# Kernel tuning notes

Hardware: AMD Instinct MI355X
Metric: run time of the kernel (lower is better)

The kernel has to match this reference:

```python
import jax, jax.numpy as jnp
import numpy as np

B, T, V, D, E = 128, 50, 10000, 512, 2048


def setup_inputs() -> dict:
    key = jax.random.key(0)
    ks = jax.random.split(key, 14)
    s = 1.0 / np.sqrt(D)
    enc_out = jax.random.normal(ks[0], (B, E), jnp.float32)
    captions = jax.random.randint(ks[1], (B, T), 0, V)
    caplens = jax.random.randint(ks[2], (B, 1), 2, T + 1)
    caplens = caplens.at[0, 0].set(T)  # ensure max(caplens)-1 == T-1 (static shape)
    return {
        "enc_out": enc_out,
        "captions": captions,
        "caplens": caplens,
        "emb_W": jax.random.normal(ks[3], (V, D), jnp.float32),
        "W_ih": jax.random.uniform(ks[4], (4 * D, D), jnp.float32, -s, s),
        "W_hh": jax.random.uniform(ks[5], (4 * D, D), jnp.float32, -s, s),
        "b_ih": jax.random.uniform(ks[6], (4 * D,), jnp.float32, -s, s),
        "b_hh": jax.random.uniform(ks[7], (4 * D,), jnp.float32, -s, s),
        "fc_W": jax.random.uniform(ks[8], (V, D), jnp.float32, -s, s),
        "fc_b": jnp.zeros((V,), jnp.float32),
        "init_h_W": jax.random.uniform(ks[9], (D, E), jnp.float32, -s, s),
        "init_h_b": jnp.zeros((D,), jnp.float32),
        "init_c_W": jax.random.uniform(ks[10], (D, E), jnp.float32, -s, s),
        "init_c_b": jnp.zeros((D,), jnp.float32),
    }


def reference(enc_out, captions, caplens, emb_W, W_ih, W_hh, b_ih, b_hh,
              fc_W, fc_b, init_h_W, init_h_b, init_c_W, init_c_b):
    # Sort by caption length, descending (manual packing in the torch code).
    cl = caplens[:, 0]
    sort_idx = jnp.argsort(-cl)
    cl = cl[sort_idx]
    enc = enc_out[sort_idx]
    caps = captions[sort_idx]

    # init_states
    h0 = enc @ init_h_W.T + init_h_b  # [B, D]
    c0 = enc @ init_c_W.T + init_c_b

    emb = emb_W[caps]                  # [B, T, D] embedding gather
    dec_lens = cl - 1                  # decode lengths, max == T-1 by construction
    Tm = caps.shape[1] - 1             # static max timesteps

    # active-row mask per timestep: row b is active at step t iff t < dec_lens[b]
    masks = jnp.arange(Tm)[:, None] < dec_lens[None, :]   # [Tm, B]
    xs = jnp.moveaxis(emb[:, :Tm, :], 1, 0)               # [Tm, B, D]

    def step(carry, inp):
        h, c = carry
        x_t, m = inp                                      # [B,D], [B]
        gates = x_t @ W_ih.T + b_ih + h @ W_hh.T + b_hh   # [B, 4D]
        i, f, g, o = jnp.split(gates, 4, axis=-1)
        i = jax.nn.sigmoid(i)
        f = jax.nn.sigmoid(f)
        g = jnp.tanh(g)
        o = jax.nn.sigmoid(o)
        c_new = f * c + i * g
        h_new = o * jnp.tanh(c_new)
        mm = m[:, None]
        # inactive (shorter) rows keep their old state; torch never touches them
        h = jnp.where(mm, h_new, h)
        c = jnp.where(mm, c_new, c)
        # dropout in eval mode == identity; preds only written for active rows
        preds = jnp.where(mm, h_new @ fc_W.T + fc_b, 0.0)  # [B, V]
        return (h, c), preds

    (_, _), preds = jax.lax.scan(step, (h0, c0), (xs, masks))  # [Tm, B, V]
    predictions = jnp.moveaxis(preds, 0, 1)                    # [B, Tm, V]
    return predictions, caps, dec_lens, sort_idx
```

## Files before the change

kernel.cpp:

```cpp
#include <hip/hip_runtime.h>
#include <hip/hip_bf16.h>
#include <math.h>

typedef __attribute__((ext_vector_type(8))) short short8;
typedef __attribute__((ext_vector_type(4))) float f32x4;
typedef __attribute__((ext_vector_type(4))) unsigned short us4;
typedef unsigned short u16;
typedef unsigned long long u64;

#define TM 49
#define NV 10000
#define NLSTM 64
#define NFC 192
#define SMEM_BYTES 133184

__device__ __forceinline__ u16 f2bf(float f) {
    union { float f; unsigned u; } v; v.f = f;
    unsigned r = v.u + 0x7fffu + ((v.u >> 16) & 1u);
    return (u16)(r >> 16);
}
__device__ __forceinline__ float fsigm(float x) {
    return 1.0f / (1.0f + __expf(-x));
}
__device__ __forceinline__ float ftanh(float x) {
    float x2 = fminf(fmaxf(x + x, -30.0f), 30.0f);
    float e = __expf(x2);
    return (e - 1.0f) / (e + 1.0f);
}

__device__ __forceinline__ short8 ld_cp128(const u16* p) {
    short8 r;
    asm volatile("global_load_dwordx4 %0, %1, off sc0 sc1" : "=v"(r) : "v"(p));
    return r;
}
__device__ __forceinline__ void st_cp16(u16* p, unsigned v) {
    asm volatile("global_store_short %0, %1, off sc0 sc1" :: "v"(p), "v"(v) : "memory");
}
__device__ __forceinline__ void st_cp32f(float* p, float v) {
    asm volatile("global_store_dword %0, %1, off sc0 sc1" :: "v"(p), "v"(v) : "memory");
}
__device__ __forceinline__ unsigned ld_cp32_wait(const unsigned* p) {
    unsigned r;
    asm volatile("global_load_dword %0, %1, off sc0 sc1\n\ts_waitcnt vmcnt(0)"
                 : "=v"(r) : "v"(p) : "memory");
    return r;
}

__global__ __launch_bounds__(128) void k_sort(
    const int* __restrict__ caplens, const int* __restrict__ captions,
    const float* __restrict__ bih, const float* __restrict__ bhh,
    int* __restrict__ sidx, int* __restrict__ decl, int* __restrict__ capsS,
    float* __restrict__ bsum, float* __restrict__ out_tail,
    unsigned* __restrict__ slots, unsigned* __restrict__ xcnt,
    int* __restrict__ offs, int* __restrict__ rowmap, int* __restrict__ maskmap)
{
    __shared__ int s_cl[128];
    __shared__ int s_si[128];
    __shared__ int s_dl[128];
    __shared__ int s_n[49];
    __shared__ int s_off[50];
    __shared__ int s_moff[128];
    int tid = threadIdx.x;
    for (int k = tid; k < 256; k += 128)
        __hip_atomic_store(&slots[k], 0u, __ATOMIC_RELAXED, __HIP_MEMORY_SCOPE_AGENT);
    for (int k = tid; k < 1568; k += 128)
        __hip_atomic_store(&xcnt[k], 0u, __ATOMIC_RELAXED, __HIP_MEMORY_SCOPE_AGENT);
    int my = caplens[tid];
    s_cl[tid] = my;
    __syncthreads();
    int r = 0;
    for (int j = 0; j < 128; j++) {
        int cj = s_cl[j];
        if (cj > my || (cj == my && j < tid)) r++;
    }
    s_si[r] = tid;
    __syncthreads();
    int src = s_si[tid];
    sidx[tid] = src;
    int dl = s_cl[src] - 1;
    decl[tid] = dl;
    s_dl[tid] = dl;
    out_tail[6400 + tid] = (float)dl;
    out_tail[6528 + tid] = (float)src;
    for (int t = 0; t < 50; t++) {
        int tok = captions[src * 50 + t];
        capsS[tid * 50 + t] = tok;
        out_tail[tid * 50 + t] = (float)tok;
    }
    for (int k = tid; k < 2048; k += 128) bsum[k] = bih[k] + bhh[k];
    __syncthreads();
    if (tid < 49) {
        int c = 0;
        for (int b = 0; b < 128; b++) c += (s_dl[b] > tid);
        s_n[tid] = c;
    }
    __syncthreads();
    if (tid == 0) {
        int a = 0;
        for (int t = 0; t < 49; t++) { s_off[t] = a; a += s_n[t]; }
        s_off[49] = a;
        int m = 0;
        for (int b = 0; b < 128; b++) { s_moff[b] = m; m += 49 - s_dl[b]; }
    }
    __syncthreads();
    if (tid < 50) offs[tid] = s_off[tid];
    for (int t = 0; t < dl; t++) rowmap[s_off[t] + tid] = t * 128 + tid;
    int mo = s_moff[tid];
    for (int t = dl; t < 49; t++) maskmap[mo + (t - dl)] = tid * 49 + t;
}

__global__ __launch_bounds__(256) void k_cvt(
    const float* __restrict__ Wih, const float* __restrict__ Whh,
    const float* __restrict__ fcW, const float* __restrict__ ihW,
    const float* __restrict__ icW,
    u16* __restrict__ WihB, u16* __restrict__ WhhB,
    u16* __restrict__ fcWB, u16* __restrict__ WhcB)
{
    int idx = blockIdx.x * 256 + threadIdx.x;
    const float* src; u16* dst; int o;
    if (idx < 262144)        { src = Wih; dst = WihB; o = idx; }
    else if (idx < 524288)   { src = Whh; dst = WhhB; o = idx - 262144; }
    else if (idx < 1804288)  { src = fcW; dst = fcWB; o = idx - 524288; }
    else if (idx < 2066432)  { src = ihW; dst = WhcB; o = idx - 1804288; }
    else                     { src = icW; dst = WhcB + 1048576; o = idx - 2066432; }
    f32x4 v = *(const f32x4*)&src[(size_t)o * 4];
    us4 b = { f2bf(v.x), f2bf(v.y), f2bf(v.z), f2bf(v.w) };
    *(us4*)&dst[(size_t)o * 4] = b;
}

__global__ __launch_bounds__(256) void k_gather(
    const float* __restrict__ enc, const float* __restrict__ embW,
    const int* __restrict__ sidx, const int* __restrict__ capsS,
    u16* __restrict__ encB, u16* __restrict__ Xemb)
{
    int idx = blockIdx.x * 256 + threadIdx.x;
    if (idx < 65536) {
        int b = idx >> 9, k4 = idx & 511;
        f32x4 v = *(const f32x4*)&enc[(size_t)sidx[b] * 2048 + k4 * 4];
        us4 o = { f2bf(v.x), f2bf(v.y), f2bf(v.z), f2bf(v.w) };
        *(us4*)&encB[(size_t)b * 2048 + k4 * 4] = o;
    } else {
        int j = idx - 65536;
        int row = j >> 7, k4 = j & 127;
        int t = row >> 7, b = row & 127;
        int tok = capsS[b * 50 + t];
        f32x4 v = *(const f32x4*)&embW[(size_t)tok * 512 + k4 * 4];
        us4 o = { f2bf(v.x), f2bf(v.y), f2bf(v.z), f2bf(v.w) };
        *(us4*)&Xemb[(size_t)row * 512 + k4 * 4] = o;
    }
}

__device__ __forceinline__ void tile_gemm_plain(
    const u16* __restrict__ A, int lda, const u16* __restrict__ B, int ldb,
    int K, int tid, u16 (*As)[40], u16 (*Bs)[40], f32x4 acc[4][4])
{
    const int w = tid >> 6, l = tid & 63;
    const int wr = (w >> 1) * 64, wc = (w & 1) * 64;
    const int lr = l & 15, lg = l >> 4;
    for (int k0 = 0; k0 < K; k0 += 32) {
        __syncthreads();
        #pragma unroll
        for (int i = 0; i < 2; i++) {
            int L = tid * 8 + i * 2048;
            int r = L >> 5, c = L & 31;
            *(short8*)&As[r][c] = *(const short8*)&A[(size_t)r * lda + k0 + c];
            *(short8*)&Bs[r][c] = *(const short8*)&B[(size_t)r * ldb + k0 + c];
        }
        __syncthreads();
        short8 af[4], bfr[4];
        #pragma unroll
        for (int m = 0; m < 4; m++) af[m] = *(const short8*)&As[wr + m * 16 + lr][lg * 8];
        #pragma unroll
        for (int n = 0; n < 4; n++) bfr[n] = *(const short8*)&Bs[wc + n * 16 + lr][lg * 8];
        #pragma unroll
        for (int m = 0; m < 4; m++)
            #pragma unroll
            for (int n = 0; n < 4; n++)
                acc[m][n] = __builtin_amdgcn_mfma_f32_16x16x32_bf16(af[m], bfr[n], acc[m][n], 0, 0, 0);
    }
}

__global__ __launch_bounds__(256, 1) void lstm_fc(
    const u16* __restrict__ Whh, float* __restrict__ X,
    u16* __restrict__ hb0, u16* __restrict__ hb1,
    u16* __restrict__ HnewC,
    const int* __restrict__ decl, unsigned* __restrict__ slots,
    unsigned* __restrict__ xcnt,
    const int* __restrict__ offs, const int* __restrict__ rowmap,
    const int* __restrict__ maskmap,
    const u16* __restrict__ fcWB, const float* __restrict__ fcb,
    const u16* __restrict__ encB, const u16* __restrict__ WhcB,
    const u16* __restrict__ WihB, const u16* __restrict__ Xemb,
    const float* __restrict__ bsum,
    const float* __restrict__ ihb, const float* __restrict__ icb,
    float* __restrict__ out)
{
    extern __shared__ char smem[];
    const int tid = threadIdx.x;
    const int wg = blockIdx.x;

    if (wg < NLSTM) {
        u16 (*As)[520] = (u16(*)[520])smem;
        u16 (*Bsi)[520] = (u16(*)[520])(smem + 33280);
        const int rb = wg >> 4, cb = wg & 15;
        const int w = tid >> 6, l = tid & 63;
        const int hi = w >> 1, lo = w & 1;
        const int lr = l & 15, lg = l >> 4;
        unsigned* cnt = slots + rb * 32;

        const int col = cb * 32 + lo * 16 + lr;
        int rowg[4];
        #pragma unroll
        for (int i = 0; i < 4; i++) rowg[i] = rb * 32 + hi * 16 + lg * 4 + i;

        f32x4 acch = {}, accc = {};
        for (int kq = 0; kq < 4; kq++) {
            __syncthreads();
            #pragma unroll
            for (int i = 0; i < 8; i++) {
                int L = tid * 8 + i * 2048;
                int r = L >> 9, cc = L & 511;
                *(short8*)&As[r][cc] =
                    *(const short8*)&encB[(size_t)(rb * 32 + r) * 2048 + kq * 512 + cc];
                *(short8*)&Bsi[r][cc] =
                    *(const short8*)&WhcB[(size_t)(cb * 32 + r) * 2048 + kq * 512 + cc];
            }
            __syncthreads();
            #pragma unroll
            for (int kk = 0; kk < 16; kk++) {
                short8 a = *(const short8*)&As[hi * 16 + lr][kk * 32 + lg * 8];
                short8 b = *(const short8*)&Bsi[lo * 16 + lr][kk * 32 + lg * 8];
                acch = __builtin_amdgcn_mfma_f32_16x16x32_bf16(a, b, acch, 0, 0, 0);
            }
            __syncthreads();
            #pragma unroll
            for (int i = 0; i < 8; i++) {
                int L = tid * 8 + i * 2048;
                int r = L >> 9, cc = L & 511;
                *(short8*)&Bsi[r][cc] =
                    *(const short8*)&WhcB[(size_t)(512 + cb * 32 + r) * 2048 + kq * 512 + cc];
            }
            __syncthreads();
            #pragma unroll
            for (int kk = 0; kk < 16; kk++) {
                short8 a = *(const short8*)&As[hi * 16 + lr][kk * 32 + lg * 8];
                short8 b = *(const short8*)&Bsi[lo * 16 + lr][kk * 32 + lg * 8];
                accc = __builtin_amdgcn_mfma_f32_16x16x32_bf16(a, b, accc, 0, 0, 0);
            }
        }

        int edec[4];
        f32x4 creg;
        us4 hreg;
        #pragma unroll
        for (int i = 0; i < 4; i++) {
            edec[i] = decl[rowg[i]];
            creg[i] = accc[i] + icb[col];
            hreg[i] = f2bf(acch[i] + ihb[col]);
            st_cp16(&hb0[(size_t)rowg[i] * 512 + col], (unsigned)hreg[i]);
        }
        asm volatile("s_waitcnt vmcnt(0)" ::: "memory");
        __syncthreads();
        if (tid == 0) atomicAdd(cnt, 1u);

        short8 bq[4][16];
        #pragma unroll
        for (int q = 0; q < 4; q++) {
            const u16* base = &Whh[(size_t)(q * 512 + cb * 32 + lo * 16 + lr) * 512 + lg * 8];
            #pragma unroll
            for (int kk = 0; kk < 16; kk++)
                bq[q][kk] = *(const short8*)&base[kk * 32];
        }
        #pragma unroll
        for (int q = 0; q < 4; q++)
            #pragma unroll
            for (int kk = 0; kk < 16; kk++)
                asm volatile("" : "+v"(bq[q][kk]));

        for (int t = 0; t < TM; t++) {
            const u16* hin = (t & 1) ? hb1 : hb0;
            u16* hout = (t & 1) ? hb0 : hb1;

            {
                unsigned tgt_h = 16u * (unsigned)(t + 1);
                if (tid == 0) {
                    while (ld_cp32_wait(cnt) < tgt_h) __builtin_amdgcn_s_sleep(1);
                } else if (tid == 64) {
                    while (ld_cp32_wait(&xcnt[t * 32]) < 16u) __builtin_amdgcn_s_sleep(1);
                }
                __syncthreads();
            }

            float xq[4][4];
            #pragma unroll
            for (int q = 0; q < 4; q++)
                #pragma unroll
                for (int i = 0; i < 4; i++)
                    xq[q][i] = X[(size_t)t * 262144 + (size_t)rowg[i] * 2048 + q * 512 + col];
            int offt = offs[t];

            short8 tmp[8];
            #pragma unroll
            for (int i = 0; i < 8; i++) {
                int L = i * 256 + tid;
                int r = L >> 6, cc = (L & 63) * 8;
                tmp[i] = ld_cp128(&hin[(size_t)(rb * 32 + r) * 512 + cc]);
            }
            asm volatile("s_waitcnt vmcnt(0)" ::: "memory");
            __builtin_amdgcn_sched_barrier(0);
            #pragma unroll
            for (int i = 0; i < 8; i++) {
                int L = i * 256 + tid;
                int r = L >> 6, cc = (L & 63) * 8;
                *(short8*)&As[r][cc] = tmp[i];
            }
            __syncthreads();

            f32x4 acc[4] = {};
            #pragma unroll
            for (int kk = 0; kk < 16; kk++) {
                short8 a = *(const short8*)&As[hi * 16 + lr][kk * 32 + lg * 8];
                acc[0] = __builtin_amdgcn_mfma_f32_16x16x32_bf16(a, bq[0][kk], acc[0], 0, 0, 0);
                acc[1] = __builtin_amdgcn_mfma_f32_16x16x32_bf16(a, bq[1][kk], acc[1], 0, 0, 0);
                acc[2] = __builtin_amdgcn_mfma_f32_16x16x32_bf16(a, bq[2][kk], acc[2], 0, 0, 0);
                acc[3] = __builtin_amdgcn_mfma_f32_16x16x32_bf16(a, bq[3][kk], acc[3], 0, 0, 0);
            }

            #pragma unroll
            for (int i = 0; i < 4; i++) {
                int act = (t < edec[i]);
                float iv = fsigm(acc[0][i] + xq[0][i]);
                float fv = fsigm(acc[1][i] + xq[1][i]);
                float gv = ftanh(acc[2][i] + xq[2][i]);
                float ov = fsigm(acc[3][i] + xq[3][i]);
                float cn = fv * creg[i] + iv * gv;
                float hn_f = ov * ftanh(cn);
                if (act) {
                    creg[i] = cn;
                    hreg[i] = f2bf(hn_f);
                }
                st_cp16(&hout[(size_t)rowg[i] * 512 + col], (unsigned)hreg[i]);
                if (act)
                    st_cp16(&HnewC[(size_t)(offt + rowg[i]) * 512 + col], (unsigned)hreg[i]);
            }

            asm volatile("s_waitcnt vmcnt(0)" ::: "memory");
            __syncthreads();
            if (tid == 0) atomicAdd(cnt, 1u);
        }
    } else {
        const int f = wg - NLSTM;
        const int w = tid >> 6, l = tid & 63;
        const int wr = (w >> 1) * 64, wc = (w & 1) * 64;
        const int lr = l & 15, lg = l >> 4;

        int nrC = offs[49];
        int nzero = 6272 - nrC;
        int nrt = (nrC + 127) >> 7;

        {
            u16 (*As)[40] = (u16(*)[40])smem;
            u16 (*Bs)[40] = (u16(*)[40])(smem + 10240);
            for (int j = f; j < 784; j += NFC) {
                int tt = j >> 4, cbx = j & 15;
                f32x4 acc[4][4] = {};
                tile_gemm_plain(Xemb + (size_t)tt * 128 * 512, 512,
                                WihB + (size_t)cbx * 128 * 512, 512,
                                512, tid, As, Bs, acc);
                #pragma unroll
                for (int m = 0; m < 4; m++)
                    #pragma unroll
                    for (int n = 0; n < 4; n++)
                        #pragma unroll
                        for (int i = 0; i < 4; i++) {
                            int row = wr + m * 16 + lg * 4 + i;
                            int colg = cbx * 128 + wc + n * 16 + lr;
                            st_cp32f(&X[(size_t)tt * 262144 + (size_t)row * 2048 + colg],
                                     acc[m][n][i] + bsum[colg]);
                        }
                asm volatile("s_waitcnt vmcnt(0)" ::: "memory");
                __syncthreads();
                if (tid == 0) atomicAdd(&xcnt[tt * 32], 1u);
            }
        }

        int c = f % 79;
        int sub = f / 79;
        int gsize = (c < 34) ? 3 : 2;

        u16 (*BT)[520] = (u16(*)[520])smem;
        unsigned* s_cnt = (unsigned*)(smem + 133120);
        __syncthreads();
        #pragma unroll
        for (int i = 0; i < 32; i++) {
            int L = i * 256 + tid;
            int r = L >> 6, cc = (L & 63) * 8;
            int gn = c * 128 + r;
            short8 b = {};
            if (gn < NV) b = *(const short8*)&fcWB[(size_t)gn * 512 + cc];
            *(short8*)&BT[r][cc] = b;
        }
        __syncthreads();

        int znext = f;
        f32x4 zv = {};

        for (int rt = sub; rt < nrt; rt += gsize) {
            int lastrow = min(rt * 128 + 127, nrC - 1);
            int tmax = rowmap[lastrow] >> 7;
            unsigned tgt = 16u * (unsigned)(tmax + 2);

            while (true) {
                if (tid < 4) s_cnt[tid] = ld_cp32_wait(slots + tid * 32);
                __syncthreads();
                bool rdy = (s_cnt[0] >= tgt) && (s_cnt[1] >= tgt) &&
                           (s_cnt[2] >= tgt) && (s_cnt[3] >= tgt);
                __syncthreads();
                if (rdy) break;
                if (znext < nzero) {
                    float* dst = out + (size_t)maskmap[znext] * 10000;
                    for (int i = tid; i < 2500; i += 256)
                        __builtin_nontemporal_store(zv, (f32x4*)&dst[i * 4]);
                    znext += NFC;
                } else {
                    __builtin_amdgcn_s_sleep(16);
                }
            }

            f32x4 acc[4][4] = {};
            #pragma unroll
            for (int ks = 0; ks < 16; ks++) {
                short8 af[4], bfr[4];
                #pragma unroll
                for (int m = 0; m < 4; m++) {
                    int gr = rt * 128 + wr + m * 16 + lr;
                    short8 a = {};
                    if (gr < nrC)
                        a = *(const short8*)&HnewC[(size_t)gr * 512 + ks * 32 + lg * 8];
                    af[m] = a;
                }
                #pragma unroll
                for (int n = 0; n < 4; n++)
                    bfr[n] = *(const short8*)&BT[wc + n * 16 + lr][ks * 32 + lg * 8];
                #pragma unroll
                for (int m = 0; m < 4; m++)
                    #pragma unroll
                    for (int n = 0; n < 4; n++)
                        acc[m][n] = __builtin_amdgcn_mfma_f32_16x16x32_bf16(af[m], bfr[n], acc[m][n], 0, 0, 0);
            }

            #pragma unroll
            for (int m = 0; m < 4; m++)
                #pragma unroll
                for (int n = 0; n < 4; n++)
                    #pragma unroll
                    for (int i = 0; i < 4; i++) {
                        int row = rt * 128 + wr + m * 16 + lg * 4 + i;
                        int colg = c * 128 + wc + n * 16 + lr;
                        if (row < nrC && colg < NV) {
                            int map = rowmap[row];
                            int b = map & 127, tt = map >> 7;
                            __builtin_nontemporal_store(
                                acc[m][n][i] + fcb[colg],
                                &out[(size_t)(b * 49 + tt) * 10000 + colg]);
                        }
                    }
        }

        while (znext < nzero) {
            float* dst = out + (size_t)maskmap[znext] * 10000;
            for (int i = tid; i < 2500; i += 256)
                __builtin_nontemporal_store(zv, (f32x4*)&dst[i * 4]);
            znext += NFC;
        }
    }
}

extern "C" void kernel_launch(void* const* d_in, const int* in_sizes, int n_in,
                              void* d_out, int out_size, void* d_ws, size_t ws_size,
                              hipStream_t stream) {
    const float* enc      = (const float*)d_in[0];
    const int*   captions = (const int*)d_in[1];
    const int*   caplens  = (const int*)d_in[2];
    const float* embW     = (const float*)d_in[3];
    const float* Wih      = (const float*)d_in[4];
    const float* Whh      = (const float*)d_in[5];
    const float* bih      = (const float*)d_in[6];
    const float* bhh      = (const float*)d_in[7];
    const float* fcW      = (const float*)d_in[8];
    const float* fcb      = (const float*)d_in[9];
    const float* ihW      = (const float*)d_in[10];
    const float* ihb      = (const float*)d_in[11];
    const float* icW      = (const float*)d_in[12];
    const float* icb      = (const float*)d_in[13];
    float* out = (float*)d_out;

    char* ws = (char*)d_ws;
    u16*   WihB = (u16*)(ws + 0);
    u16*   WhhB = (u16*)(ws + 2097152);
    u16*   fcWB = (u16*)(ws + 4194304);
    u16*   WhcB = (u16*)(ws + 14434304);
    u16*   encB = (u16*)(ws + 18628608);
    u16*   Xemb = (u16*)(ws + 19152896);
    float* X    = (float*)(ws + 25575424);
    u16*   HnewC= (u16*)(ws + 76955648);
    u16*   hb0  = (u16*)(ws + 83378176);
    u16*   hb1  = (u16*)(ws + 83509248);
    int*   sidx = (int*)(ws + 83902464);
    int*   decl = (int*)(ws + 83902976);
    int*   capsS= (int*)(ws + 83903488);
    float* bsum = (float*)(ws + 83929088);
    unsigned* slots = (unsigned*)(ws + 83937280);
    int*   offs   = (int*)(ws + 83938304);
    int*   rowmap = (int*)(ws + 83938560);
    int*   maskmap= (int*)(ws + 83963648);
    unsigned* xcnt = (unsigned*)(ws + 83988736);

    k_sort<<<1, 128, 0, stream>>>(caplens, captions, bih, bhh, sidx, decl, capsS, bsum,
                                  out + 62720000, slots, xcnt, offs, rowmap, maskmap);
    k_cvt<<<9096, 256, 0, stream>>>(Wih, Whh, fcW, ihW, icW, WihB, WhhB, fcWB, WhcB);
    k_gather<<<3392, 256, 0, stream>>>(enc, embW, sidx, capsS, encB, Xemb);
    lstm_fc<<<NLSTM + NFC, 256, SMEM_BYTES, stream>>>(
        WhhB, X, hb0, hb1, HnewC, decl, slots, xcnt, offs, rowmap, maskmap,
        fcWB, fcb, encB, WhcB, WihB, Xemb, bsum, ihb, icb, out);
}
```

Before: 350.2 us.

## Replace atomic step counters with per-workgroup flags polled in parallel

```diff
diff --git a/kernel.cpp b/kernel.cpp
--- a/kernel.cpp
+++ b/kernel.cpp
@@ -39,6 +39,9 @@
 __device__ __forceinline__ void st_cp32f(float* p, float v) {
     asm volatile("global_store_dword %0, %1, off sc0 sc1" :: "v"(p), "v"(v) : "memory");
 }
+__device__ __forceinline__ void st_cp32u(unsigned* p, unsigned v) {
+    asm volatile("global_store_dword %0, %1, off sc0 sc1" :: "v"(p), "v"(v) : "memory");
+}
 __device__ __forceinline__ unsigned ld_cp32_wait(const unsigned* p) {
     unsigned r;
     asm volatile("global_load_dword %0, %1, off sc0 sc1\n\ts_waitcnt vmcnt(0)"
@@ -51,7 +54,7 @@
     const float* __restrict__ bih, const float* __restrict__ bhh,
     int* __restrict__ sidx, int* __restrict__ decl, int* __restrict__ capsS,
     float* __restrict__ bsum, float* __restrict__ out_tail,
-    unsigned* __restrict__ slots, unsigned* __restrict__ xcnt,
+    unsigned* __restrict__ flags, unsigned* __restrict__ xcnt,
     int* __restrict__ offs, int* __restrict__ rowmap, int* __restrict__ maskmap)
 {
     __shared__ int s_cl[128];
@@ -61,8 +64,8 @@
     __shared__ int s_off[50];
     __shared__ int s_moff[128];
     int tid = threadIdx.x;
-    for (int k = tid; k < 256; k += 128)
-        __hip_atomic_store(&slots[k], 0u, __ATOMIC_RELAXED, __HIP_MEMORY_SCOPE_AGENT);
+    for (int k = tid; k < 2048; k += 128)
+        __hip_atomic_store(&flags[k], 0u, __ATOMIC_RELAXED, __HIP_MEMORY_SCOPE_AGENT);
     for (int k = tid; k < 1568; k += 128)
         __hip_atomic_store(&xcnt[k], 0u, __ATOMIC_RELAXED, __HIP_MEMORY_SCOPE_AGENT);
     int my = caplens[tid];
@@ -184,7 +187,7 @@
     const u16* __restrict__ Whh, float* __restrict__ X,
     u16* __restrict__ hb0, u16* __restrict__ hb1,
     u16* __restrict__ HnewC,
-    const int* __restrict__ decl, unsigned* __restrict__ slots,
+    const int* __restrict__ decl, unsigned* __restrict__ flags,
     unsigned* __restrict__ xcnt,
     const int* __restrict__ offs, const int* __restrict__ rowmap,
     const int* __restrict__ maskmap,
@@ -206,7 +209,7 @@
         const int w = tid >> 6, l = tid & 63;
         const int hi = w >> 1, lo = w & 1;
         const int lr = l & 15, lg = l >> 4;
-        unsigned* cnt = slots + rb * 32;
+        unsigned* myflag = &flags[(rb * 16 + cb) * 32];
 
         const int col = cb * 32 + lo * 16 + lr;
         int rowg[4];
@@ -261,7 +264,7 @@
         }
         asm volatile("s_waitcnt vmcnt(0)" ::: "memory");
         __syncthreads();
-        if (tid == 0) atomicAdd(cnt, 1u);
+        if (tid == 0) st_cp32u(myflag, 1u);
 
         short8 bq[4][16];
         #pragma unroll
@@ -281,15 +284,18 @@
             const u16* hin = (t & 1) ? hb1 : hb0;
             u16* hout = (t & 1) ? hb0 : hb1;
 
-            {
-                unsigned tgt_h = 16u * (unsigned)(t + 1);
-                if (tid == 0) {
-                    while (ld_cp32_wait(cnt) < tgt_h) __builtin_amdgcn_s_sleep(1);
-                } else if (tid == 64) {
-                    while (ld_cp32_wait(&xcnt[t * 32]) < 16u) __builtin_amdgcn_s_sleep(1);
+            if (tid < 64) {
+                unsigned tgt_h = (unsigned)(t + 1);
+                while (true) {
+                    bool ok = true;
+                    if (tid < 16)
+                        ok = (ld_cp32_wait(&flags[(rb * 16 + tid) * 32]) >= tgt_h);
+                    else if (tid == 16)
+                        ok = (ld_cp32_wait(&xcnt[t * 32]) >= 16u);
+                    if (__all(ok)) break;
                 }
-                __syncthreads();
-            }
+            }
+            __syncthreads();
 
             float xq[4][4];
             #pragma unroll
@@ -340,14 +346,20 @@
                     hreg[i] = f2bf(hn_f);
                 }
                 st_cp16(&hout[(size_t)rowg[i] * 512 + col], (unsigned)hreg[i]);
-                if (act)
+            }
+
+            asm volatile("s_waitcnt vmcnt(0)" ::: "memory");
+            __syncthreads();
+            if (tid == 0) st_cp32u(myflag, (unsigned)(t + 2));
+            #pragma unroll
+            for (int i = 0; i < 4; i++)
+                if (t < edec[i])
                     st_cp16(&HnewC[(size_t)(offt + rowg[i]) * 512 + col], (unsigned)hreg[i]);
-            }
-
-            asm volatile("s_waitcnt vmcnt(0)" ::: "memory");
-            __syncthreads();
-            if (tid == 0) atomicAdd(cnt, 1u);
-        }
+        }
+
+        asm volatile("s_waitcnt vmcnt(0)" ::: "memory");
+        __syncthreads();
+        if (tid == 0) st_cp32u(myflag, (unsigned)(TM + 2));
     } else {
         const int f = wg - NLSTM;
         const int w = tid >> 6, l = tid & 63;
@@ -389,7 +401,7 @@
         int gsize = (c < 34) ? 3 : 2;
 
         u16 (*BT)[520] = (u16(*)[520])smem;
-        unsigned* s_cnt = (unsigned*)(smem + 133120);
+        unsigned* s_rdy = (unsigned*)(smem + 133120);
         __syncthreads();
         #pragma unroll
         for (int i = 0; i < 32; i++) {
@@ -408,13 +420,14 @@
         for (int rt = sub; rt < nrt; rt += gsize) {
             int lastrow = min(rt * 128 + 127, nrC - 1);
             int tmax = rowmap[lastrow] >> 7;
-            unsigned tgt = 16u * (unsigned)(tmax + 2);
+            unsigned tgt = (unsigned)(tmax + 3);
 
             while (true) {
-                if (tid < 4) s_cnt[tid] = ld_cp32_wait(slots + tid * 32);
+                bool ok = (tid < 64) ? (ld_cp32_wait(&flags[tid * 32]) >= tgt) : true;
+                int allv = __all(ok);
+                if (tid == 0) *s_rdy = (unsigned)allv;
                 __syncthreads();
-                bool rdy = (s_cnt[0] >= tgt) && (s_cnt[1] >= tgt) &&
-                           (s_cnt[2] >= tgt) && (s_cnt[3] >= tgt);
+                bool rdy = (*s_rdy != 0);
                 __syncthreads();
                 if (rdy) break;
                 if (znext < nzero) {
@@ -423,7 +436,7 @@
                         __builtin_nontemporal_store(zv, (f32x4*)&dst[i * 4]);
                     znext += NFC;
                 } else {
-                    __builtin_amdgcn_s_sleep(16);
+                    __builtin_amdgcn_s_sleep(32);
                 }
             }
 
@@ -506,21 +519,21 @@
     u16*   HnewC= (u16*)(ws + 76955648);
     u16*   hb0  = (u16*)(ws + 83378176);
     u16*   hb1  = (u16*)(ws + 83509248);
+    unsigned* flags = (unsigned*)(ws + 83640320);
     int*   sidx = (int*)(ws + 83902464);
     int*   decl = (int*)(ws + 83902976);
     int*   capsS= (int*)(ws + 83903488);
     float* bsum = (float*)(ws + 83929088);
-    unsigned* slots = (unsigned*)(ws + 83937280);
     int*   offs   = (int*)(ws + 83938304);
     int*   rowmap = (int*)(ws + 83938560);
     int*   maskmap= (int*)(ws + 83963648);
     unsigned* xcnt = (unsigned*)(ws + 83988736);
 
     k_sort<<<1, 128, 0, stream>>>(caplens, captions, bih, bhh, sidx, decl, capsS, bsum,
-                                  out + 62720000, slots, xcnt, offs, rowmap, maskmap);
+                                  out + 62720000, flags, xcnt, offs, rowmap, maskmap);
     k_cvt<<<9096, 256, 0, stream>>>(Wih, Whh, fcW, ihW, icW, WihB, WhhB, fcWB, WhcB);
     k_gather<<<3392, 256, 0, stream>>>(enc, embW, sidx, capsS, encB, Xemb);
     lstm_fc<<<NLSTM + NFC, 256, SMEM_BYTES, stream>>>(
-        WhhB, X, hb0, hb1, HnewC, decl, slots, xcnt, offs, rowmap, maskmap,
+        WhhB, X, hb0, hb1, HnewC, decl, flags, xcnt, offs, rowmap, maskmap,
         fcWB, fcb, encB, WhcB, WihB, Xemb, bsum, ihb, icb, out);
 }
```

New measurement: 332.1 us. 5.2% less time.
